# Performance work log

Hardware: AMD Instinct MI355X
Metric: run time of the kernel (lower is better)

Reference implementation:

```python
import jax, jax.numpy as jnp
import numpy as np

BETA = 2.0  # init kwarg beta


def _roi_map(roi_params, H, W):
    # roi_params: (N, K, 4) = (mu_x, mu_y, sigma_x, sigma_y) in [0, 1]
    dtype = roi_params.dtype
    gx = (jnp.arange(W, dtype=dtype) + 0.5) / W  # x-coords of grid columns
    gy = (jnp.arange(H, dtype=dtype) + 0.5) / H  # y-coords of grid rows
    mu_x, mu_y = roi_params[:, :, 0], roi_params[:, :, 1]
    sg_x, sg_y = roi_params[:, :, 2], roi_params[:, :, 3]
    # separable generalized-Gaussian log pdf along each axis
    log_x = -(jnp.abs(gx[None, None, :] - mu_x[:, :, None]) / sg_x[:, :, None]) ** BETA  # (N,K,W)
    log_y = -(jnp.abs(gy[None, None, :] - mu_y[:, :, None]) / sg_y[:, :, None]) ** BETA  # (N,K,H)
    scores = jnp.exp(log_y[:, :, :, None] + log_x[:, :, None, :])  # (N,K,H,W)
    mx = jnp.max(scores, axis=(2, 3), keepdims=True)
    return scores / (mx + 1e-12)  # max-normalized attention maps


def setup_inputs() -> dict:
    key = jax.random.key(0)
    k1, k2 = jax.random.split(key)
    x = jax.random.normal(k1, (16, 128, 128, 256), dtype=jnp.float32)
    roi_params = jax.random.uniform(k2, (16, 64, 4), dtype=jnp.float32)
    return {"x": x, "roi_params": roi_params}


def reference(x, roi_params):
    N, H, W, d = x.shape
    roi_map = _roi_map(roi_params, H, W)           # (N,K,H,W)
    flat_map = roi_map.reshape(N, -1, H * W)        # (N,K,HW)
    flat_feats = x.reshape(N, H * W, d)             # (N,HW,d)
    roi_features = jnp.einsum('nrf,nfd->nrd', flat_map, flat_feats) / (H * W)
    return roi_features, roi_params, roi_map
```

## Files before the change

### kernel.cpp

```cpp
#include <hip/hip_runtime.h>
#include <hip/hip_bf16.h>
#include <math.h>

#define NB 16
#define RB 64
#define HB 128
#define WB 128
#define DB 256
#define HW (HB * WB)

typedef __attribute__((ext_vector_type(8))) short bf16x8;
typedef __attribute__((ext_vector_type(4))) short short4v;
typedef __attribute__((ext_vector_type(4))) float f32x4;

static __device__ __forceinline__ short f2bf(float f) {
  __hip_bfloat16 h = __float2bfloat16(f);
  return *reinterpret_cast<short*>(&h);
}
static __device__ __forceinline__ float bf2f(short s) {
  return __uint_as_float(((unsigned)(unsigned short)s) << 16);
}

#define GLOAD_LDS16(gp, lp)                                          \
  __builtin_amdgcn_global_load_lds(                                  \
      (const __attribute__((address_space(1))) unsigned int*)(gp),   \
      (__attribute__((address_space(3))) unsigned int*)(lp), 16, 0, 0)

static __device__ __forceinline__ float axis_maxlog(float mu, float sg) {
  int i = (int)roundf(mu * 128.0f - 0.5f);
  i = i < 0 ? 0 : (i > 127 ? 127 : i);
  const float g = (i + 0.5f) * (1.0f / 128.0f);
  const float tm = fabsf(g - mu) / sg;
  return -(tm * tm);
}

template <bool WMAP>
__global__ __launch_bounds__(512, 1) void fused_kernel(
    const float* __restrict__ x, const float* __restrict__ roi,
    short* __restrict__ partials, float* __restrict__ out_map) {
  __shared__ float buf[4][32 * DB];

  const int bid = blockIdx.x;
  const int n   = bid >> 4;
  const int kc  = bid & 15;
  const int t   = threadIdx.x;
  const int l   = t & 63;
  const int wv  = t >> 6;
  const int mh  = wv >> 2;
  const int dw  = wv & 3;
  const int l15 = l & 15;
  const int lk  = (l >> 4) * 8;
  const int h0  = kc * 8;
  const int dbase = dw * 64 + l15 * 4;

  const char* gx =
      (const char*)(x + ((size_t)n * HW + (size_t)kc * 1024) * DB);
  char* lbase = (char*)&buf[0][0];

  f32x4 exr[2][4][2];
  float eyv[8][2];
#pragma unroll
  for (int rf = 0; rf < 2; ++rf) {
    const int nr = n * RB + mh * 32 + rf * 16 + l15;
    const float4 rp = reinterpret_cast<const float4*>(roi)[nr];
    const float mlx = axis_maxlog(rp.x, rp.z);
    const float mly = axis_maxlog(rp.y, rp.w);
    const float em  = expf(mlx + mly);
    const float s   = em / (em + 1e-12f);
#pragma unroll
    for (int ks = 0; ks < 4; ++ks) {
#pragma unroll
      for (int hf = 0; hf < 2; ++hf) {
        f32x4 v;
#pragma unroll
        for (int j = 0; j < 4; ++j) {
          const int col = ks * 32 + lk + hf * 4 + j;
          const float g = (col + 0.5f) * (1.0f / 128.0f);
          const float tx = fabsf(g - rp.x) / rp.z;
          v[j] = expf(-(tx * tx) - mlx);
        }
        exr[rf][ks][hf] = v;
      }
    }
#pragma unroll
    for (int hh = 0; hh < 8; ++hh) {
      const float g = (h0 + hh + 0.5f) * (1.0f / 128.0f);
      const float ty = fabsf(g - rp.y) / rp.w;
      eyv[hh][rf] = expf(-(ty * ty) - mly) * s;
    }
  }
  asm volatile("s_waitcnt vmcnt(0)" ::: "memory");

  f32x4 acc[2][4];
#pragma unroll
  for (int rf = 0; rf < 2; ++rf)
#pragma unroll
    for (int f = 0; f < 4; ++f) acc[rf][f] = (f32x4)0.0f;

#define STAGE(bi, slot) do {                                                 \
    const char* gsrc_ = gx + (size_t)(bi) * 32768;                           \
    char* ldst_ = lbase + (slot) * 32768;                                    \
    _Pragma("unroll")                                                        \
    for (int ii = 0; ii < 4; ++ii)                                           \
      GLOAD_LDS16(gsrc_ + ii * 8192 + wv * 1024 + l * 16,                    \
                  ldst_ + ii * 8192 + wv * 1024);                            \
  } while (0)

  STAGE(0, 0); STAGE(1, 1); STAGE(2, 2);

#define KSTEP(bi, VM, DO_STAGE) do {                                         \
    asm volatile("s_waitcnt vmcnt(" #VM ")" ::: "memory");                   \
    __builtin_amdgcn_s_barrier();                                            \
    __builtin_amdgcn_sched_barrier(0);                                       \
    if (DO_STAGE) STAGE((bi) + 3, ((bi) + 3) & 3);                           \
    const float* bp_ = &buf[(bi) & 3][0];                                    \
    f32x4 xv_[8];                                                            \
    _Pragma("unroll")                                                        \
    for (int j = 0; j < 8; ++j)                                              \
      xv_[j] = *reinterpret_cast<const f32x4*>(                              \
          bp_ + (lk + j) * DB + dbase);                                      \
    bf16x8 bfr_[4];                                                          \
    _Pragma("unroll")                                                        \
    for (int f = 0; f < 4; ++f) {                                            \
      bf16x8 b_;                                                             \
      _Pragma("unroll")                                                      \
      for (int j = 0; j < 8; ++j) b_[j] = f2bf(xv_[j][f]);                   \
      bfr_[f] = b_;                                                          \
    }                                                                        \
    bf16x8 afr_[2];                                                          \
    _Pragma("unroll")                                                        \
    for (int rf = 0; rf < 2; ++rf) {                                         \
      const float ey_ = eyv[(bi) >> 2][rf];                                  \
      const f32x4 e0_ = exr[rf][(bi) & 3][0];                                \
      const f32x4 e1_ = exr[rf][(bi) & 3][1];                                \
      bf16x8 a_;                                                             \
      a_[0] = f2bf(ey_ * e0_.x); a_[1] = f2bf(ey_ * e0_.y);                  \
      a_[2] = f2bf(ey_ * e0_.z); a_[3] = f2bf(ey_ * e0_.w);                  \
      a_[4] = f2bf(ey_ * e1_.x); a_[5] = f2bf(ey_ * e1_.y);                  \
      a_[6] = f2bf(ey_ * e1_.z); a_[7] = f2bf(ey_ * e1_.w);                  \
      afr_[rf] = a_;                                                         \
    }                                                                        \
    _Pragma("unroll")                                                        \
    for (int rf = 0; rf < 2; ++rf)                                           \
      _Pragma("unroll")                                                      \
      for (int f = 0; f < 4; ++f)                                            \
        acc[rf][f] = __builtin_amdgcn_mfma_f32_16x16x32_bf16(                \
            afr_[rf], bfr_[f], acc[rf][f], 0, 0, 0);                         \
  } while (0)

  KSTEP(0, 8, 1);   KSTEP(1, 8, 1);   KSTEP(2, 8, 1);   KSTEP(3, 8, 1);
  KSTEP(4, 8, 1);   KSTEP(5, 8, 1);   KSTEP(6, 8, 1);   KSTEP(7, 8, 1);
  KSTEP(8, 8, 1);   KSTEP(9, 8, 1);   KSTEP(10, 8, 1);  KSTEP(11, 8, 1);
  KSTEP(12, 8, 1);  KSTEP(13, 8, 1);  KSTEP(14, 8, 1);  KSTEP(15, 8, 1);
  KSTEP(16, 8, 1);  KSTEP(17, 8, 1);  KSTEP(18, 8, 1);  KSTEP(19, 8, 1);
  KSTEP(20, 8, 1);  KSTEP(21, 8, 1);  KSTEP(22, 8, 1);  KSTEP(23, 8, 1);
  KSTEP(24, 8, 1);  KSTEP(25, 8, 1);  KSTEP(26, 8, 1);  KSTEP(27, 8, 1);
  KSTEP(28, 8, 1);  KSTEP(29, 8, 0);  KSTEP(30, 4, 0);  KSTEP(31, 0, 0);

#undef KSTEP
#undef STAGE

  short* P = partials + (size_t)bid * (RB * DB);
#pragma unroll
  for (int rf = 0; rf < 2; ++rf) {
#pragma unroll
    for (int reg = 0; reg < 4; ++reg) {
      const int r = mh * 32 + rf * 16 + (l >> 4) * 4 + reg;
      short4v v;
      v.x = f2bf(acc[rf][0][reg]); v.y = f2bf(acc[rf][1][reg]);
      v.z = f2bf(acc[rf][2][reg]); v.w = f2bf(acc[rf][3][reg]);
      *reinterpret_cast<short4v*>(P + (size_t)r * DB + dbase) = v;
    }
  }

  if constexpr (WMAP) {
    const int h  = h0 + wv;
    const int p4 = l & 31;
    const float gh = (h + 0.5f) * (1.0f / 128.0f);
#pragma unroll 4
    for (int it = 0; it < 32; ++it) {
      const int r = it * 2 + (l >> 5);
      const float4 rp = reinterpret_cast<const float4*>(roi)[n * RB + r];
      const float mlx = axis_maxlog(rp.x, rp.z);
      const float mly = axis_maxlog(rp.y, rp.w);
      const float em  = expf(mlx + mly);
      const float s   = em / (em + 1e-12f);
      const float ty  = fabsf(gh - rp.y) / rp.w;
      const float ey  = expf(-(ty * ty) - mly) * s;
      f32x4 v;
#pragma unroll
      for (int j = 0; j < 4; ++j) {
        const float g  = (p4 * 4 + j + 0.5f) * (1.0f / 128.0f);
        const float tx = fabsf(g - rp.x) / rp.z;
        v[j] = expf(-(tx * tx) - mlx) * ey;
      }
      *reinterpret_cast<f32x4*>(
          out_map + ((size_t)(n * RB + r) * HB + h) * WB + p4 * 4) = v;
    }
  }
}

__global__ __launch_bounds__(512) void map_only_kernel(
    const float* __restrict__ roi, float* __restrict__ out_map) {
  __shared__ float sT[1024];
  const int mb = blockIdx.x;
  const int t  = threadIdx.x;
  float* sEx = sT;
  float* sEy = sT + 512;
  for (int v = t; v < 1024; v += 512) {
    const int rr = v >> 8, axis = (v >> 7) & 1, pos = v & 127;
    const float4 rp = reinterpret_cast<const float4*>(roi)[mb * 4 + rr];
    const float mlx = axis_maxlog(rp.x, rp.z);
    const float mly = axis_maxlog(rp.y, rp.w);
    const float em  = expf(mlx + mly);
    const float s   = em / (em + 1e-12f);
    const float g   = (pos + 0.5f) * (1.0f / 128.0f);
    if (axis == 0) {
      const float tx = fabsf(g - rp.x) / rp.z;
      sEx[rr * 128 + pos] = expf(-(tx * tx) - mlx);
    } else {
      const float ty = fabsf(g - rp.y) / rp.w;
      sEy[rr * 128 + pos] = expf(-(ty * ty) - mly) * s;
    }
  }
  __syncthreads();
  f32x4* dst = reinterpret_cast<f32x4*>(out_map + (size_t)mb * 4 * HW);
#pragma unroll
  for (int p = 0; p < 32; ++p) {
    const int idx = p * 512 + t;
    const int rr = idx >> 12, h = (idx >> 5) & 127, w4 = idx & 31;
    const f32x4 e = *reinterpret_cast<const f32x4*>(&sEx[rr * 128 + w4 * 4]);
    dst[idx] = e * (f32x4)sEy[rr * 128 + h];
  }
}

__global__ __launch_bounds__(256) void reduce_kernel(
    const short* __restrict__ partials, const float* __restrict__ roi,
    float* __restrict__ outF, float* __restrict__ out_params) {
  const int idx = blockIdx.x * 256 + threadIdx.x;
  const int n   = idx >> 12;
  const int i4  = idx & 4095;
  const short4v* p =
      reinterpret_cast<const short4v*>(partials) + (size_t)n * 16 * 4096 + i4;
  f32x4 s = (f32x4)0.0f;
#pragma unroll
  for (int kc = 0; kc < 16; ++kc) {
    const short4v v = p[(size_t)kc * 4096];
    s.x += bf2f(v.x); s.y += bf2f(v.y); s.z += bf2f(v.z); s.w += bf2f(v.w);
  }
  s *= (1.0f / (float)HW);
  reinterpret_cast<f32x4*>(outF)[idx] = s;
  if (idx < NB * RB * 4) out_params[idx] = roi[idx];
}

extern "C" void kernel_launch(void* const* d_in, const int* in_sizes, int n_in,
                              void* d_out, int out_size, void* d_ws, size_t ws_size,
                              hipStream_t stream) {
  const float* x   = (const float*)d_in[0];
  const float* roi = (const float*)d_in[1];
  float* out        = (float*)d_out;
  float* out_feat   = out;
  float* out_params = out + NB * RB * DB;
  float* out_map    = out_params + NB * RB * 4;

  const size_t par_shorts = 256u * RB * DB;
  const bool ws_ok = ws_size >= par_shorts * sizeof(short) + 64;

  if (ws_ok) {
    short* P = (short*)d_ws;
    fused_kernel<true><<<256, 512, 0, stream>>>(x, roi, P, out_map);
    reduce_kernel<<<256, 256, 0, stream>>>(P, roi, out_feat, out_params);
  } else {
    short* P = (short*)out_map;
    fused_kernel<false><<<256, 512, 0, stream>>>(x, roi, P, out_map);
    reduce_kernel<<<256, 256, 0, stream>>>(P, roi, out_feat, out_params);
    map_only_kernel<<<256, 512, 0, stream>>>(roi, out_map);
  }
}
```

Baseline: 94.92 us.

## Split map writing out of feature kernel, halve K-chunk, use register-staged double buffer

The fused kernel is replaced by a feature-only kernel that launches 512 blocks, each covering 4 rows (512 pixels), instead of 256 blocks of 8 rows. It uses a 2-slot LDS buffer filled through registers rather than a 4-slot global_load_lds ring, and recomputes the x-axis Gaussian weights inline instead of keeping them in registers. Smaller LDS and register use aim to allow more resident blocks for better latency hiding and wave balance. The attention map is now always written by the separate map_only_kernel, and the reduction sums 32 partials. The cost is more partial traffic, one extra launch, extra exp work per step, and a simpler pipeline with a barrier every step.

```diff
diff --git a/kernel.cpp b/kernel.cpp
--- a/kernel.cpp
+++ b/kernel.cpp
@@ -21,11 +21,6 @@
   return __uint_as_float(((unsigned)(unsigned short)s) << 16);
 }
 
-#define GLOAD_LDS16(gp, lp)                                          \
-  __builtin_amdgcn_global_load_lds(                                  \
-      (const __attribute__((address_space(1))) unsigned int*)(gp),   \
-      (__attribute__((address_space(3))) unsigned int*)(lp), 16, 0, 0)
-
 static __device__ __forceinline__ float axis_maxlog(float mu, float sg) {
   int i = (int)roundf(mu * 128.0f - 0.5f);
   i = i < 0 ? 0 : (i > 127 ? 127 : i);
@@ -34,15 +29,14 @@
   return -(tm * tm);
 }
 
-template <bool WMAP>
-__global__ __launch_bounds__(512, 1) void fused_kernel(
+__global__ __launch_bounds__(512, 4) void feat_kernel(
     const float* __restrict__ x, const float* __restrict__ roi,
-    short* __restrict__ partials, float* __restrict__ out_map) {
-  __shared__ float buf[4][32 * DB];
+    short* __restrict__ partials) {
+  __shared__ float buf[2][32 * DB];
 
   const int bid = blockIdx.x;
-  const int n   = bid >> 4;
-  const int kc  = bid & 15;
+  const int n   = bid >> 5;
+  const int kc  = bid & 31;
   const int t   = threadIdx.x;
   const int l   = t & 63;
   const int wv  = t >> 6;
@@ -50,46 +44,31 @@
   const int dw  = wv & 3;
   const int l15 = l & 15;
   const int lk  = (l >> 4) * 8;
-  const int h0  = kc * 8;
+  const int h0  = kc * 4;
   const int dbase = dw * 64 + l15 * 4;
 
-  const char* gx =
-      (const char*)(x + ((size_t)n * HW + (size_t)kc * 1024) * DB);
-  char* lbase = (char*)&buf[0][0];
-
-  f32x4 exr[2][4][2];
-  float eyv[8][2];
+  const f32x4* gx4 =
+      reinterpret_cast<const f32x4*>(x + ((size_t)n * HW + (size_t)kc * 512) * DB);
+
+  float mux[2], c2x[2], mlx[2];
+  float eyv[4][2];
 #pragma unroll
   for (int rf = 0; rf < 2; ++rf) {
     const int nr = n * RB + mh * 32 + rf * 16 + l15;
     const float4 rp = reinterpret_cast<const float4*>(roi)[nr];
-    const float mlx = axis_maxlog(rp.x, rp.z);
-    const float mly = axis_maxlog(rp.y, rp.w);
-    const float em  = expf(mlx + mly);
-    const float s   = em / (em + 1e-12f);
-#pragma unroll
-    for (int ks = 0; ks < 4; ++ks) {
-#pragma unroll
-      for (int hf = 0; hf < 2; ++hf) {
-        f32x4 v;
-#pragma unroll
-        for (int j = 0; j < 4; ++j) {
-          const int col = ks * 32 + lk + hf * 4 + j;
-          const float g = (col + 0.5f) * (1.0f / 128.0f);
-          const float tx = fabsf(g - rp.x) / rp.z;
-          v[j] = expf(-(tx * tx) - mlx);
-        }
-        exr[rf][ks][hf] = v;
-      }
-    }
-#pragma unroll
-    for (int hh = 0; hh < 8; ++hh) {
+    const float mlx_ = axis_maxlog(rp.x, rp.z);
+    const float mly_ = axis_maxlog(rp.y, rp.w);
+    const float em   = expf(mlx_ + mly_);
+    const float s    = em / (em + 1e-12f);
+    const float isx  = 1.0f / rp.z;
+    mux[rf] = rp.x; c2x[rf] = isx * isx; mlx[rf] = mlx_;
+#pragma unroll
+    for (int hh = 0; hh < 4; ++hh) {
       const float g = (h0 + hh + 0.5f) * (1.0f / 128.0f);
       const float ty = fabsf(g - rp.y) / rp.w;
-      eyv[hh][rf] = expf(-(ty * ty) - mly) * s;
+      eyv[hh][rf] = expf(-(ty * ty) - mly_) * s;
     }
   }
-  asm volatile("s_waitcnt vmcnt(0)" ::: "memory");
 
   f32x4 acc[2][4];
 #pragma unroll
@@ -97,23 +76,25 @@
 #pragma unroll
     for (int f = 0; f < 4; ++f) acc[rf][f] = (f32x4)0.0f;
 
-#define STAGE(bi, slot) do {                                                 \
-    const char* gsrc_ = gx + (size_t)(bi) * 32768;                           \
-    char* ldst_ = lbase + (slot) * 32768;                                    \
-    _Pragma("unroll")                                                        \
-    for (int ii = 0; ii < 4; ++ii)                                           \
-      GLOAD_LDS16(gsrc_ + ii * 8192 + wv * 1024 + l * 16,                    \
-                  ldst_ + ii * 8192 + wv * 1024);                            \
+  f32x4 g0, g1, g2, g3;
+#define GLOAD(bi) do {                                                       \
+    const f32x4* gp_ = gx4 + (size_t)(bi) * 2048;                            \
+    g0 = gp_[t]; g1 = gp_[t + 512]; g2 = gp_[t + 1024]; g3 = gp_[t + 1536];  \
   } while (0)
-
-  STAGE(0, 0); STAGE(1, 1); STAGE(2, 2);
-
-#define KSTEP(bi, VM, DO_STAGE) do {                                         \
-    asm volatile("s_waitcnt vmcnt(" #VM ")" ::: "memory");                   \
-    __builtin_amdgcn_s_barrier();                                            \
-    __builtin_amdgcn_sched_barrier(0);                                       \
-    if (DO_STAGE) STAGE((bi) + 3, ((bi) + 3) & 3);                           \
-    const float* bp_ = &buf[(bi) & 3][0];                                    \
+#define DSWRITE(slot) do {                                                   \
+    f32x4* lp_ = reinterpret_cast<f32x4*>(&buf[slot][0]);                    \
+    lp_[t] = g0; lp_[t + 512] = g1; lp_[t + 1024] = g2; lp_[t + 1536] = g3;  \
+  } while (0)
+
+  GLOAD(0);
+  DSWRITE(0);
+  asm volatile("s_waitcnt lgkmcnt(0)" ::: "memory");
+  __builtin_amdgcn_s_barrier();
+  __builtin_amdgcn_sched_barrier(0);
+
+#define KSTEP(bi) do {                                                       \
+    if ((bi) < 15) GLOAD((bi) + 1);                                          \
+    const float* bp_ = &buf[(bi) & 1][0];                                    \
     f32x4 xv_[8];                                                            \
     _Pragma("unroll")                                                        \
     for (int j = 0; j < 8; ++j)                                              \
@@ -131,13 +112,15 @@
     _Pragma("unroll")                                                        \
     for (int rf = 0; rf < 2; ++rf) {                                         \
       const float ey_ = eyv[(bi) >> 2][rf];                                  \
-      const f32x4 e0_ = exr[rf][(bi) & 3][0];                                \
-      const f32x4 e1_ = exr[rf][(bi) & 3][1];                                \
       bf16x8 a_;                                                             \
-      a_[0] = f2bf(ey_ * e0_.x); a_[1] = f2bf(ey_ * e0_.y);                  \
-      a_[2] = f2bf(ey_ * e0_.z); a_[3] = f2bf(ey_ * e0_.w);                  \
-      a_[4] = f2bf(ey_ * e1_.x); a_[5] = f2bf(ey_ * e1_.y);                  \
-      a_[6] = f2bf(ey_ * e1_.z); a_[7] = f2bf(ey_ * e1_.w);                  \
+      _Pragma("unroll")                                                      \
+      for (int i = 0; i < 8; ++i) {                                          \
+        const int col = ((bi) & 3) * 32 + lk + i;                            \
+        const float g_ = (col + 0.5f) * (1.0f / 128.0f);                     \
+        const float d_ = g_ - mux[rf];                                       \
+        const float e_ = expf(-(d_ * d_ * c2x[rf]) - mlx[rf]);               \
+        a_[i] = f2bf(ey_ * e_);                                              \
+      }                                                                      \
       afr_[rf] = a_;                                                         \
     }                                                                        \
     _Pragma("unroll")                                                        \
@@ -146,19 +129,20 @@
       for (int f = 0; f < 4; ++f)                                            \
         acc[rf][f] = __builtin_amdgcn_mfma_f32_16x16x32_bf16(                \
             afr_[rf], bfr_[f], acc[rf][f], 0, 0, 0);                         \
+    if ((bi) < 15) DSWRITE(((bi) + 1) & 1);                                  \
+    asm volatile("s_waitcnt lgkmcnt(0)" ::: "memory");                       \
+    __builtin_amdgcn_s_barrier();                                            \
+    __builtin_amdgcn_sched_barrier(0);                                       \
   } while (0)
 
-  KSTEP(0, 8, 1);   KSTEP(1, 8, 1);   KSTEP(2, 8, 1);   KSTEP(3, 8, 1);
-  KSTEP(4, 8, 1);   KSTEP(5, 8, 1);   KSTEP(6, 8, 1);   KSTEP(7, 8, 1);
-  KSTEP(8, 8, 1);   KSTEP(9, 8, 1);   KSTEP(10, 8, 1);  KSTEP(11, 8, 1);
-  KSTEP(12, 8, 1);  KSTEP(13, 8, 1);  KSTEP(14, 8, 1);  KSTEP(15, 8, 1);
-  KSTEP(16, 8, 1);  KSTEP(17, 8, 1);  KSTEP(18, 8, 1);  KSTEP(19, 8, 1);
-  KSTEP(20, 8, 1);  KSTEP(21, 8, 1);  KSTEP(22, 8, 1);  KSTEP(23, 8, 1);
-  KSTEP(24, 8, 1);  KSTEP(25, 8, 1);  KSTEP(26, 8, 1);  KSTEP(27, 8, 1);
-  KSTEP(28, 8, 1);  KSTEP(29, 8, 0);  KSTEP(30, 4, 0);  KSTEP(31, 0, 0);
+  KSTEP(0);  KSTEP(1);  KSTEP(2);  KSTEP(3);
+  KSTEP(4);  KSTEP(5);  KSTEP(6);  KSTEP(7);
+  KSTEP(8);  KSTEP(9);  KSTEP(10); KSTEP(11);
+  KSTEP(12); KSTEP(13); KSTEP(14); KSTEP(15);
 
 #undef KSTEP
-#undef STAGE
+#undef DSWRITE
+#undef GLOAD
 
   short* P = partials + (size_t)bid * (RB * DB);
 #pragma unroll
@@ -170,32 +154,6 @@
       v.x = f2bf(acc[rf][0][reg]); v.y = f2bf(acc[rf][1][reg]);
       v.z = f2bf(acc[rf][2][reg]); v.w = f2bf(acc[rf][3][reg]);
       *reinterpret_cast<short4v*>(P + (size_t)r * DB + dbase) = v;
-    }
-  }
-
-  if constexpr (WMAP) {
-    const int h  = h0 + wv;
-    const int p4 = l & 31;
-    const float gh = (h + 0.5f) * (1.0f / 128.0f);
-#pragma unroll 4
-    for (int it = 0; it < 32; ++it) {
-      const int r = it * 2 + (l >> 5);
-      const float4 rp = reinterpret_cast<const float4*>(roi)[n * RB + r];
-      const float mlx = axis_maxlog(rp.x, rp.z);
-      const float mly = axis_maxlog(rp.y, rp.w);
-      const float em  = expf(mlx + mly);
-      const float s   = em / (em + 1e-12f);
-      const float ty  = fabsf(gh - rp.y) / rp.w;
-      const float ey  = expf(-(ty * ty) - mly) * s;
-      f32x4 v;
-#pragma unroll
-      for (int j = 0; j < 4; ++j) {
-        const float g  = (p4 * 4 + j + 0.5f) * (1.0f / 128.0f);
-        const float tx = fabsf(g - rp.x) / rp.z;
-        v[j] = expf(-(tx * tx) - mlx) * ey;
-      }
-      *reinterpret_cast<f32x4*>(
-          out_map + ((size_t)(n * RB + r) * HB + h) * WB + p4 * 4) = v;
     }
   }
 }
@@ -241,10 +199,10 @@
   const int n   = idx >> 12;
   const int i4  = idx & 4095;
   const short4v* p =
-      reinterpret_cast<const short4v*>(partials) + (size_t)n * 16 * 4096 + i4;
+      reinterpret_cast<const short4v*>(partials) + (size_t)n * 32 * 4096 + i4;
   f32x4 s = (f32x4)0.0f;
 #pragma unroll
-  for (int kc = 0; kc < 16; ++kc) {
+  for (int kc = 0; kc < 32; ++kc) {
     const short4v v = p[(size_t)kc * 4096];
     s.x += bf2f(v.x); s.y += bf2f(v.y); s.z += bf2f(v.z); s.w += bf2f(v.w);
   }
@@ -263,17 +221,12 @@
   float* out_params = out + NB * RB * DB;
   float* out_map    = out_params + NB * RB * 4;
 
-  const size_t par_shorts = 256u * RB * DB;
+  const size_t par_shorts = 512u * RB * DB;
   const bool ws_ok = ws_size >= par_shorts * sizeof(short) + 64;
 
-  if (ws_ok) {
-    short* P = (short*)d_ws;
-    fused_kernel<true><<<256, 512, 0, stream>>>(x, roi, P, out_map);
-    reduce_kernel<<<256, 256, 0, stream>>>(P, roi, out_feat, out_params);
-  } else {
-    short* P = (short*)out_map;
-    fused_kernel<false><<<256, 512, 0, stream>>>(x, roi, P, out_map);
-    reduce_kernel<<<256, 256, 0, stream>>>(P, roi, out_feat, out_params);
-    map_only_kernel<<<256, 512, 0, stream>>>(roi, out_map);
-  }
-}
+  short* P = ws_ok ? (short*)d_ws : (short*)out_map;
+
+  feat_kernel<<<512, 512, 0, stream>>>(x, roi, P);
+  reduce_kernel<<<256, 256, 0, stream>>>(P, roi, out_feat, out_params);
+  map_only_kernel<<<256, 512, 0, stream>>>(roi, out_map);
+}
```

New measurement: 99.62 us. 5.0% more time.
